# Kernel tuning notes

Hardware: AMD Instinct MI355X
Metric: run time of the kernel (lower is better)

The kernel has to match this reference:

```python
import jax, jax.numpy as jnp
import numpy as np

C = 5          # max within-cluster spike gap (module-level constant in source repo)
DELTA = 0.05   # margin constant (module-level constant in source repo)
B, T, N = 128, 512, 256


def setup_inputs() -> dict:
    key = jax.random.key(0)
    k1, k2, k3 = jax.random.split(key, 3)
    vmem = jax.random.normal(k1, (B, T, N), dtype=jnp.float32) - 1.5
    vlastmem = jax.random.normal(k2, (B, T, N), dtype=jnp.float32)  # unused by the loss math
    labels_t = jax.random.randint(k3, (B, N), 0, 4)
    ratio = jnp.float32(0.5)
    return {"vmem": vmem, "vlastmem": vlastmem, "labels_t": labels_t, "ratio": ratio}


def _per_neuron(v, key):
    """v: [T] membrane trace for one (batch, neuron). Returns (num_cluster, under_term, max_over)."""
    Tn = v.shape[0]
    t = jnp.arange(Tn)
    spike = v >= 0.0
    s = spike.astype(jnp.int32)
    # prefix sums: cs[i] = number of spikes in v[:i]
    cs = jnp.concatenate([jnp.zeros(1, jnp.int32), jnp.cumsum(s)])
    # new cluster starts at t iff spike[t] and no spike in [t-C, t-1]  (gap > C)
    prev_cnt = cs[t] - cs[jnp.clip(t - C, 0, Tn)]
    is_start = spike & (prev_cnt == 0)
    nclu = jnp.sum(is_start.astype(jnp.int32))
    # under-branch mask = union over clusters of [first-C, last+C] = C-dilation of spike train
    dil_cnt = cs[jnp.clip(t + C + 1, 0, Tn)] - cs[jnp.clip(t - C, 0, Tn)]
    mask = dil_cnt > 0

    # per-cluster stats via segmented reductions (cluster id = running count of starts)
    cid = jnp.clip(jnp.cumsum(is_start.astype(jnp.int32)) - 1, 0, Tn - 1)
    counts = jax.ops.segment_sum(s, cid, num_segments=Tn)
    first = jax.ops.segment_min(jnp.where(spike, t, Tn), cid, num_segments=Tn)
    last = jax.ops.segment_max(jnp.where(spike, t, -1), cid, num_segments=Tn)

    # over branch: cluster minimizing (end_idx - beg_idx) == min spike count (first on ties)
    counts_q = jnp.where(t < nclu, counts, Tn + 2)
    ic = jnp.argmin(counts_q)
    over_mask = (t >= first[ic]) & (t <= last[ic])
    max_over = jnp.max(jnp.where(over_mask, v, -jnp.inf))

    # under branch: if unmasked timesteps remain, penalize -max(v[mask==0]);
    # else take v at a (pinned-seed) random spike position
    has_zero = jnp.any(~mask)
    max_unmask = jnp.max(jnp.where(~mask, v, -jnp.inf))
    nsp = cs[-1]
    sorted_pos = jnp.sort(jnp.where(spike, t, Tn))
    r = jax.random.randint(key, (), 0, jnp.maximum(nsp, 1))
    v_rand = v[jnp.clip(sorted_pos[r], 0, Tn - 1)]
    under_term = jnp.where(has_zero, -max_unmask, v_rand)
    return nclu, under_term, max_over


def _forward(vmem, vlastmem, labels_t, ratio):
    Bv, Tv, Nv = vmem.shape
    vflat = jnp.swapaxes(vmem, 1, 2).reshape(Bv * Nv, Tv)   # [B*N, T]
    lflat = labels_t.reshape(Bv * Nv)
    keys = jax.random.split(jax.random.key(42), Bv * Nv)     # pinned seed for the random-spike pick
    nclu, under_term, max_over = jax.vmap(_per_neuron)(vflat, keys)
    ncf = nclu.astype(vmem.dtype)
    margin = DELTA * ratio * ncf
    under = jnp.where(lflat > nclu, under_term + margin, 0.0)
    over = jnp.where(lflat < nclu, max_over + margin, 0.0)
    loss = jnp.sum(under + over)
    spike_output = ncf.reshape(Bv, Nv)
    return loss, spike_output


def reference(vmem, vlastmem, labels_t, ratio):
    return _forward(vmem, vlastmem, labels_t, ratio)
```

## Files before the change

kernel.cpp:

```cpp
#include <hip/hip_runtime.h>
#include <stdint.h>

#define TDIM 512
#define NDIM 256
#define CGAP 5
#define DELTA_C 0.05f
#define NSEG 16
#define SEGT 32
#define BIGI (1 << 28)

extern "C" __global__ void __launch_bounds__(1024, 8)
stca_kernel(const float* __restrict__ vmem, const int* __restrict__ labels,
            const float* __restrict__ ratio_p, float* __restrict__ out,
            float* __restrict__ ws) {
  __shared__ int   si[8][NSEG * 64];
  __shared__ float sf[6][NSEG * 64];

  const int lane = threadIdx.x & 63;
  const int seg  = threadIdx.x >> 6;
  const int blk  = blockIdx.x;
  const int b    = blk >> 2;
  const int n0   = (blk & 3) << 6;
  const int n    = n0 + lane;

  const float* g = vmem + (size_t)b * TDIM * NDIM + n;
  const int t0 = seg * SEGT, t1 = t0 + SEGT;

  int   last_spike = -1000, nclu = 0, cur_cnt = 0, cur_fs = 0, fs = BIGI;
  float cur_max = -INFINITY, cur_maxlast = -INFINITY;
  float seg_run_max = -INFINITY, mfs_snap = -INFINITY;
  int   pfx_cnt = 0, pfx_ls = 0;
  float pfx_core = -INFINITY, pfx_mfs = -INFINITY;
  int   bint_cnt = BIGI;
  float bint_max = -INFINITY;
  unsigned hist = 0u;
  float umax = -INFINITY;
  float vd0 = 0.f, vd1 = 0.f, vd2 = 0.f, vd3 = 0.f, vd4 = 0.f, vd5 = 0.f;

  if (t0 > 0) {
#pragma unroll
    for (int j = 0; j < CGAP; ++j) {
      const float v = g[(size_t)(t0 - CGAP + j) * NDIM];
      hist = ((hist << 1) | (v >= 0.f ? 1u : 0u)) & 0x7FFu;
    }
  }

  auto step = [&](float v, int te) {
    const bool spike   = v >= 0.0f;
    const bool isstart = spike && ((te - last_spike) > CGAP);
    const bool closing = isstart && (nclu > 0);
    const bool isfirst = closing && (nclu == 1);
    const bool bet     = closing && (nclu > 1) && (cur_cnt < bint_cnt);
    pfx_cnt  = isfirst ? cur_cnt     : pfx_cnt;
    pfx_ls   = isfirst ? last_spike  : pfx_ls;
    pfx_core = isfirst ? cur_maxlast : pfx_core;
    pfx_mfs  = isfirst ? mfs_snap    : pfx_mfs;
    bint_cnt = bet ? cur_cnt     : bint_cnt;
    bint_max = bet ? cur_maxlast : bint_max;
    nclu += isstart ? 1 : 0;
    cur_fs  = isstart ? te : cur_fs;
    cur_max = isstart ? v : fmaxf(cur_max, v);
    cur_maxlast = spike ? cur_max : cur_maxlast;
    cur_cnt = (isstart ? 0 : cur_cnt) + (spike ? 1 : 0);
    seg_run_max = fmaxf(seg_run_max, v);
    const bool snap = spike && (nclu == 1);
    mfs_snap = snap ? seg_run_max : mfs_snap;
    fs = (spike && fs == BIGI) ? te : fs;
    last_spike = spike ? te : last_spike;
    hist = ((hist << 1) | (spike ? 1u : 0u)) & 0x7FFu;
    vd5 = vd4; vd4 = vd3; vd3 = vd2; vd2 = vd1; vd1 = vd0; vd0 = v;
    const bool un = (hist == 0u) && (te >= t0 + CGAP);
    umax = un ? fmaxf(umax, vd5) : umax;
  };

#pragma unroll 1
  for (int c = 0; c < SEGT / 8; ++c) {
    const float* gp = g + (size_t)(t0 + c * 8) * NDIM;
    const float y0 = gp[0 * NDIM], y1 = gp[1 * NDIM], y2 = gp[2 * NDIM],
                y3 = gp[3 * NDIM], y4 = gp[4 * NDIM], y5 = gp[5 * NDIM],
                y6 = gp[6 * NDIM], y7 = gp[7 * NDIM];
    const int tc = t0 + c * 8;
    step(y0, tc + 0); step(y1, tc + 1); step(y2, tc + 2); step(y3, tc + 3);
    step(y4, tc + 4); step(y5, tc + 5); step(y6, tc + 6); step(y7, tc + 7);
  }

#pragma unroll
  for (int j = 0; j < CGAP; ++j) {
    const int te = t1 + j;
    const float v = (te < TDIM) ? g[(size_t)te * NDIM] : -INFINITY;
    const bool spike = v >= 0.0f;
    hist = ((hist << 1) | (spike ? 1u : 0u)) & 0x7FFu;
    vd5 = vd4; vd4 = vd3; vd3 = vd2; vd2 = vd1; vd1 = vd0; vd0 = v;
    const bool un = (hist == 0u);
    umax = un ? fmaxf(umax, vd5) : umax;
  }

  int   sfx_cnt = 0, sfx_fs = 0;
  float sfx_core = -INFINITY, sfx_mte = -INFINITY;
  if (nclu >= 1) {
    sfx_cnt = cur_cnt; sfx_fs = cur_fs; sfx_core = cur_maxlast; sfx_mte = cur_max;
    if (nclu == 1) {
      pfx_cnt = cur_cnt; pfx_ls = last_spike; pfx_core = cur_maxlast; pfx_mfs = mfs_snap;
    }
  }

  const int idx = threadIdx.x;
  si[0][idx] = nclu;    si[1][idx] = fs;      si[2][idx] = last_spike;
  si[3][idx] = pfx_cnt; si[4][idx] = pfx_ls;  si[5][idx] = sfx_cnt;
  si[6][idx] = sfx_fs;  si[7][idx] = bint_cnt;
  sf[0][idx] = pfx_core; sf[1][idx] = pfx_mfs; sf[2][idx] = sfx_core;
  sf[3][idx] = sfx_mte;  sf[4][idx] = bint_max; sf[5][idx] = umax;
  __syncthreads();

  if (seg != 0) return;

  int   a_nclu = nclu, a_fs = fs, a_ls = last_spike;
  int   a_pcnt = pfx_cnt, a_pls = pfx_ls, a_scnt = sfx_cnt, a_sfs = sfx_fs;
  int   a_bcnt = bint_cnt;
  float a_pcore = pfx_core, a_pmfs = pfx_mfs, a_score = sfx_core, a_smte = sfx_mte;
  float a_bmax = bint_max, a_umax = umax;

  for (int s = 1; s < NSEG; ++s) {
    const int j = (s << 6) + lane;
    const int   r_nclu = si[0][j], r_fs = si[1][j], r_ls = si[2][j];
    const int   r_pcnt = si[3][j], r_pls = si[4][j];
    const int   r_scnt = si[5][j], r_sfs = si[6][j];
    const int   r_bcnt = si[7][j];
    const float r_pcore = sf[0][j], r_pmfs = sf[1][j];
    const float r_score = sf[2][j], r_smte = sf[3][j];
    const float r_bmax = sf[4][j], r_umax = sf[5][j];

    a_umax = fmaxf(a_umax, r_umax);
    if (r_nclu == 0) continue;
    if (a_nclu == 0) {
      a_nclu = r_nclu; a_fs = r_fs; a_ls = r_ls;
      a_pcnt = r_pcnt; a_pls = r_pls; a_pcore = r_pcore; a_pmfs = r_pmfs;
      a_scnt = r_scnt; a_sfs = r_sfs; a_score = r_score; a_smte = r_smte;
      a_bcnt = r_bcnt; a_bmax = r_bmax;
      continue;
    }
    if (r_fs - a_ls <= CGAP) {
      const int   Bc    = a_scnt + r_pcnt;
      const float Bcore = fmaxf(a_smte, r_pmfs);
      const float Bmfs  = fmaxf(fmaxf(a_pmfs, a_smte), r_pmfs);
      const float Bmte  = fmaxf(fmaxf(a_smte, r_pmfs), r_smte);
      const int   Bfs = a_sfs, Bls = r_pls;
      int nb = a_bcnt; float nbm = a_bmax;
      if (a_nclu >= 2 && r_nclu >= 2 && Bc < nb) { nb = Bc; nbm = Bcore; }
      if (r_bcnt < nb) { nb = r_bcnt; nbm = r_bmax; }
      if (a_nclu == 1) { a_pcnt = Bc; a_pls = Bls; a_pcore = Bcore; a_pmfs = Bmfs; }
      if (r_nclu == 1) { a_scnt = Bc; a_sfs = Bfs; a_score = Bcore; a_smte = Bmte; }
      else             { a_scnt = r_scnt; a_sfs = r_sfs; a_score = r_score; a_smte = r_smte; }
      a_bcnt = nb; a_bmax = nbm;
      a_nclu = a_nclu + r_nclu - 1;
      a_ls = r_ls;
    } else {
      int nb = a_bcnt; float nbm = a_bmax;
      if (a_nclu >= 2 && a_scnt < nb) { nb = a_scnt; nbm = a_score; }
      if (r_nclu >= 2 && r_pcnt < nb) { nb = r_pcnt; nbm = r_pcore; }
      if (r_bcnt < nb) { nb = r_bcnt; nbm = r_bmax; }
      a_bcnt = nb; a_bmax = nbm;
      a_scnt = r_scnt; a_sfs = r_sfs; a_score = r_score; a_smte = r_smte;
      a_nclu += r_nclu;
      a_ls = r_ls;
    }
  }

  int bc = a_pcnt; float bm = a_pcore;
  if (a_nclu >= 2) {
    if (a_bcnt < bc) { bc = a_bcnt; bm = a_bmax; }
    if (a_scnt < bc) { bc = a_scnt; bm = a_score; }
  }

  const float ratio = ratio_p[0];
  const int   label = labels[b * NDIM + n];
  const float ncf    = (float)a_nclu;
  const float margin = DELTA_C * ratio * ncf;
  const float under_term = (a_umax > -INFINITY) ? (-a_umax) : 0.0f;
  const float under = (label > a_nclu) ? (under_term + margin) : 0.0f;
  const float over  = (label < a_nclu) ? (bm + margin) : 0.0f;

  out[1 + b * NDIM + n] = ncf;

  float sum = under + over;
#pragma unroll
  for (int off = 32; off > 0; off >>= 1) sum += __shfl_down(sum, off);
  if (lane == 0) ws[blk] = sum;
}

extern "C" __global__ void __launch_bounds__(64, 1)
stca_reduce(const float* __restrict__ ws, float* __restrict__ out) {
  const int lane = threadIdx.x;
  float s = 0.0f;
#pragma unroll
  for (int i = 0; i < 8; ++i) s += ws[lane + (i << 6)];
#pragma unroll
  for (int off = 32; off > 0; off >>= 1) s += __shfl_down(s, off);
  if (lane == 0) out[0] = s;
}

extern "C" void kernel_launch(void* const* d_in, const int* in_sizes, int n_in,
                              void* d_out, int out_size, void* d_ws,
                              size_t ws_size, hipStream_t stream) {
  const float* vmem   = (const float*)d_in[0];
  const int*   labels = (const int*)d_in[2];
  const float* ratio  = (const float*)d_in[3];
  float* out = (float*)d_out;
  float* ws  = (float*)d_ws;

  dim3 grid(512);
  dim3 block(1024);
  hipLaunchKernelGGL(stca_kernel, grid, block, 0, stream, vmem, labels, ratio,
                     out, ws);
  hipLaunchKernelGGL(stca_reduce, dim3(1), dim3(64), 0, stream, ws, out);
}
```

Baseline: 168.5 us.

## Process two time segments per thread with interleaved independent scans

Each thread now runs two independent segment scans (A and B) with their steps interleaved, and the block shrinks from 1024 to 512 threads. The goal is more instruction-level parallelism and more loads in flight per thread on the serial dependency chain, plus less per-block shared-memory traffic and work in the merge, since segment B is merged straight from registers. The cost is higher register pressure from two scan states, which may reduce occupancy.

```diff
diff --git a/kernel.cpp b/kernel.cpp
--- a/kernel.cpp
+++ b/kernel.cpp
@@ -9,7 +9,85 @@
 #define SEGT 32
 #define BIGI (1 << 28)
 
-extern "C" __global__ void __launch_bounds__(1024, 8)
+struct Scan {
+  int   last_spike, nclu, cur_cnt, cur_fs, fs;
+  float cur_max, cur_maxlast, seg_run_max, mfs_snap;
+  int   pfx_cnt, pfx_ls;
+  float pfx_core, pfx_mfs;
+  int   bint_cnt;
+  float bint_max;
+  unsigned hist;
+  float umax;
+  float vd0, vd1, vd2, vd3, vd4, vd5;
+};
+
+__device__ __forceinline__ void scan_init(Scan& S) {
+  S.last_spike = -1000; S.nclu = 0; S.cur_cnt = 0; S.cur_fs = 0; S.fs = BIGI;
+  S.cur_max = -INFINITY; S.cur_maxlast = -INFINITY;
+  S.seg_run_max = -INFINITY; S.mfs_snap = -INFINITY;
+  S.pfx_cnt = 0; S.pfx_ls = 0; S.pfx_core = -INFINITY; S.pfx_mfs = -INFINITY;
+  S.bint_cnt = BIGI; S.bint_max = -INFINITY;
+  S.hist = 0u; S.umax = -INFINITY;
+  S.vd0 = S.vd1 = S.vd2 = S.vd3 = S.vd4 = S.vd5 = 0.f;
+}
+
+__device__ __forceinline__ void scan_step(Scan& S, float v, int te, int t0) {
+  const bool spike   = v >= 0.0f;
+  const bool isstart = spike && ((te - S.last_spike) > CGAP);
+  const bool closing = isstart && (S.nclu > 0);
+  const bool isfirst = closing && (S.nclu == 1);
+  const bool bet     = closing && (S.nclu > 1) && (S.cur_cnt < S.bint_cnt);
+  S.pfx_cnt  = isfirst ? S.cur_cnt     : S.pfx_cnt;
+  S.pfx_ls   = isfirst ? S.last_spike  : S.pfx_ls;
+  S.pfx_core = isfirst ? S.cur_maxlast : S.pfx_core;
+  S.pfx_mfs  = isfirst ? S.mfs_snap    : S.pfx_mfs;
+  S.bint_cnt = bet ? S.cur_cnt     : S.bint_cnt;
+  S.bint_max = bet ? S.cur_maxlast : S.bint_max;
+  S.nclu += isstart ? 1 : 0;
+  S.cur_fs  = isstart ? te : S.cur_fs;
+  S.cur_max = isstart ? v : fmaxf(S.cur_max, v);
+  S.cur_maxlast = spike ? S.cur_max : S.cur_maxlast;
+  S.cur_cnt = (isstart ? 0 : S.cur_cnt) + (spike ? 1 : 0);
+  S.seg_run_max = fmaxf(S.seg_run_max, v);
+  const bool snap = spike && (S.nclu == 1);
+  S.mfs_snap = snap ? S.seg_run_max : S.mfs_snap;
+  S.fs = (spike && S.fs == BIGI) ? te : S.fs;
+  S.last_spike = spike ? te : S.last_spike;
+  S.hist = ((S.hist << 1) | (spike ? 1u : 0u)) & 0x7FFu;
+  S.vd5 = S.vd4; S.vd4 = S.vd3; S.vd3 = S.vd2; S.vd2 = S.vd1; S.vd1 = S.vd0;
+  S.vd0 = v;
+  const bool un = (S.hist == 0u) && (te >= t0 + CGAP);
+  S.umax = un ? fmaxf(S.umax, S.vd5) : S.umax;
+}
+
+__device__ __forceinline__ void scan_post(Scan& S, const float* g, int t1) {
+#pragma unroll
+  for (int j = 0; j < CGAP; ++j) {
+    const int te = t1 + j;
+    const float v = (te < TDIM) ? g[(size_t)te * NDIM] : -INFINITY;
+    const bool spike = v >= 0.0f;
+    S.hist = ((S.hist << 1) | (spike ? 1u : 0u)) & 0x7FFu;
+    S.vd5 = S.vd4; S.vd4 = S.vd3; S.vd3 = S.vd2; S.vd2 = S.vd1; S.vd1 = S.vd0;
+    S.vd0 = v;
+    const bool un = (S.hist == 0u);
+    S.umax = un ? fmaxf(S.umax, S.vd5) : S.umax;
+  }
+}
+
+__device__ __forceinline__ void scan_final(Scan& S, int& sfx_cnt, int& sfx_fs,
+                                           float& sfx_core, float& sfx_mte) {
+  sfx_cnt = 0; sfx_fs = 0; sfx_core = -INFINITY; sfx_mte = -INFINITY;
+  if (S.nclu >= 1) {
+    sfx_cnt = S.cur_cnt; sfx_fs = S.cur_fs;
+    sfx_core = S.cur_maxlast; sfx_mte = S.cur_max;
+    if (S.nclu == 1) {
+      S.pfx_cnt = S.cur_cnt; S.pfx_ls = S.last_spike;
+      S.pfx_core = S.cur_maxlast; S.pfx_mfs = S.mfs_snap;
+    }
+  }
+}
+
+extern "C" __global__ void __launch_bounds__(512, 4)
 stca_kernel(const float* __restrict__ vmem, const int* __restrict__ labels,
             const float* __restrict__ ratio_p, float* __restrict__ out,
             float* __restrict__ ws) {
@@ -24,120 +102,88 @@
   const int n    = n0 + lane;
 
   const float* g = vmem + (size_t)b * TDIM * NDIM + n;
-  const int t0 = seg * SEGT, t1 = t0 + SEGT;
-
-  int   last_spike = -1000, nclu = 0, cur_cnt = 0, cur_fs = 0, fs = BIGI;
-  float cur_max = -INFINITY, cur_maxlast = -INFINITY;
-  float seg_run_max = -INFINITY, mfs_snap = -INFINITY;
-  int   pfx_cnt = 0, pfx_ls = 0;
-  float pfx_core = -INFINITY, pfx_mfs = -INFINITY;
-  int   bint_cnt = BIGI;
-  float bint_max = -INFINITY;
-  unsigned hist = 0u;
-  float umax = -INFINITY;
-  float vd0 = 0.f, vd1 = 0.f, vd2 = 0.f, vd3 = 0.f, vd4 = 0.f, vd5 = 0.f;
-
-  if (t0 > 0) {
+  const int sA = seg << 1, sB = sA + 1;
+  const int t0A = sA * SEGT, t0B = sB * SEGT;
+
+  Scan A, B;
+  scan_init(A); scan_init(B);
+
+  if (t0A > 0) {
 #pragma unroll
     for (int j = 0; j < CGAP; ++j) {
-      const float v = g[(size_t)(t0 - CGAP + j) * NDIM];
-      hist = ((hist << 1) | (v >= 0.f ? 1u : 0u)) & 0x7FFu;
-    }
-  }
-
-  auto step = [&](float v, int te) {
-    const bool spike   = v >= 0.0f;
-    const bool isstart = spike && ((te - last_spike) > CGAP);
-    const bool closing = isstart && (nclu > 0);
-    const bool isfirst = closing && (nclu == 1);
-    const bool bet     = closing && (nclu > 1) && (cur_cnt < bint_cnt);
-    pfx_cnt  = isfirst ? cur_cnt     : pfx_cnt;
-    pfx_ls   = isfirst ? last_spike  : pfx_ls;
-    pfx_core = isfirst ? cur_maxlast : pfx_core;
-    pfx_mfs  = isfirst ? mfs_snap    : pfx_mfs;
-    bint_cnt = bet ? cur_cnt     : bint_cnt;
-    bint_max = bet ? cur_maxlast : bint_max;
-    nclu += isstart ? 1 : 0;
-    cur_fs  = isstart ? te : cur_fs;
-    cur_max = isstart ? v : fmaxf(cur_max, v);
-    cur_maxlast = spike ? cur_max : cur_maxlast;
-    cur_cnt = (isstart ? 0 : cur_cnt) + (spike ? 1 : 0);
-    seg_run_max = fmaxf(seg_run_max, v);
-    const bool snap = spike && (nclu == 1);
-    mfs_snap = snap ? seg_run_max : mfs_snap;
-    fs = (spike && fs == BIGI) ? te : fs;
-    last_spike = spike ? te : last_spike;
-    hist = ((hist << 1) | (spike ? 1u : 0u)) & 0x7FFu;
-    vd5 = vd4; vd4 = vd3; vd3 = vd2; vd2 = vd1; vd1 = vd0; vd0 = v;
-    const bool un = (hist == 0u) && (te >= t0 + CGAP);
-    umax = un ? fmaxf(umax, vd5) : umax;
-  };
+      const float v = g[(size_t)(t0A - CGAP + j) * NDIM];
+      A.hist = ((A.hist << 1) | (v >= 0.f ? 1u : 0u)) & 0x7FFu;
+    }
+  }
+#pragma unroll
+  for (int j = 0; j < CGAP; ++j) {
+    const float v = g[(size_t)(t0B - CGAP + j) * NDIM];
+    B.hist = ((B.hist << 1) | (v >= 0.f ? 1u : 0u)) & 0x7FFu;
+  }
 
 #pragma unroll 1
   for (int c = 0; c < SEGT / 8; ++c) {
-    const float* gp = g + (size_t)(t0 + c * 8) * NDIM;
-    const float y0 = gp[0 * NDIM], y1 = gp[1 * NDIM], y2 = gp[2 * NDIM],
-                y3 = gp[3 * NDIM], y4 = gp[4 * NDIM], y5 = gp[5 * NDIM],
-                y6 = gp[6 * NDIM], y7 = gp[7 * NDIM];
-    const int tc = t0 + c * 8;
-    step(y0, tc + 0); step(y1, tc + 1); step(y2, tc + 2); step(y3, tc + 3);
-    step(y4, tc + 4); step(y5, tc + 5); step(y6, tc + 6); step(y7, tc + 7);
-  }
-
-#pragma unroll
-  for (int j = 0; j < CGAP; ++j) {
-    const int te = t1 + j;
-    const float v = (te < TDIM) ? g[(size_t)te * NDIM] : -INFINITY;
-    const bool spike = v >= 0.0f;
-    hist = ((hist << 1) | (spike ? 1u : 0u)) & 0x7FFu;
-    vd5 = vd4; vd4 = vd3; vd3 = vd2; vd2 = vd1; vd1 = vd0; vd0 = v;
-    const bool un = (hist == 0u);
-    umax = un ? fmaxf(umax, vd5) : umax;
-  }
-
-  int   sfx_cnt = 0, sfx_fs = 0;
-  float sfx_core = -INFINITY, sfx_mte = -INFINITY;
-  if (nclu >= 1) {
-    sfx_cnt = cur_cnt; sfx_fs = cur_fs; sfx_core = cur_maxlast; sfx_mte = cur_max;
-    if (nclu == 1) {
-      pfx_cnt = cur_cnt; pfx_ls = last_spike; pfx_core = cur_maxlast; pfx_mfs = mfs_snap;
-    }
-  }
-
-  const int idx = threadIdx.x;
-  si[0][idx] = nclu;    si[1][idx] = fs;      si[2][idx] = last_spike;
-  si[3][idx] = pfx_cnt; si[4][idx] = pfx_ls;  si[5][idx] = sfx_cnt;
-  si[6][idx] = sfx_fs;  si[7][idx] = bint_cnt;
-  sf[0][idx] = pfx_core; sf[1][idx] = pfx_mfs; sf[2][idx] = sfx_core;
-  sf[3][idx] = sfx_mte;  sf[4][idx] = bint_max; sf[5][idx] = umax;
+    const float* gpA = g + (size_t)(t0A + c * 8) * NDIM;
+    const float* gpB = g + (size_t)(t0B + c * 8) * NDIM;
+    const float y0 = gpA[0 * NDIM], y1 = gpA[1 * NDIM], y2 = gpA[2 * NDIM],
+                y3 = gpA[3 * NDIM], y4 = gpA[4 * NDIM], y5 = gpA[5 * NDIM],
+                y6 = gpA[6 * NDIM], y7 = gpA[7 * NDIM];
+    const float z0 = gpB[0 * NDIM], z1 = gpB[1 * NDIM], z2 = gpB[2 * NDIM],
+                z3 = gpB[3 * NDIM], z4 = gpB[4 * NDIM], z5 = gpB[5 * NDIM],
+                z6 = gpB[6 * NDIM], z7 = gpB[7 * NDIM];
+    const int ta = t0A + c * 8, tb = t0B + c * 8;
+    scan_step(A, y0, ta + 0, t0A); scan_step(B, z0, tb + 0, t0B);
+    scan_step(A, y1, ta + 1, t0A); scan_step(B, z1, tb + 1, t0B);
+    scan_step(A, y2, ta + 2, t0A); scan_step(B, z2, tb + 2, t0B);
+    scan_step(A, y3, ta + 3, t0A); scan_step(B, z3, tb + 3, t0B);
+    scan_step(A, y4, ta + 4, t0A); scan_step(B, z4, tb + 4, t0B);
+    scan_step(A, y5, ta + 5, t0A); scan_step(B, z5, tb + 5, t0B);
+    scan_step(A, y6, ta + 6, t0A); scan_step(B, z6, tb + 6, t0B);
+    scan_step(A, y7, ta + 7, t0A); scan_step(B, z7, tb + 7, t0B);
+  }
+
+  scan_post(A, g, t0A + SEGT);
+  scan_post(B, g, t0B + SEGT);
+
+  int sfxA_cnt, sfxA_fs; float sfxA_core, sfxA_mte;
+  int sfxB_cnt, sfxB_fs; float sfxB_core, sfxB_mte;
+  scan_final(A, sfxA_cnt, sfxA_fs, sfxA_core, sfxA_mte);
+  scan_final(B, sfxB_cnt, sfxB_fs, sfxB_core, sfxB_mte);
+
+  const int iA = (sA << 6) + lane, iB = (sB << 6) + lane;
+  si[0][iA] = A.nclu;    si[1][iA] = A.fs;      si[2][iA] = A.last_spike;
+  si[3][iA] = A.pfx_cnt; si[4][iA] = A.pfx_ls;  si[5][iA] = sfxA_cnt;
+  si[6][iA] = sfxA_fs;   si[7][iA] = A.bint_cnt;
+  sf[0][iA] = A.pfx_core; sf[1][iA] = A.pfx_mfs; sf[2][iA] = sfxA_core;
+  sf[3][iA] = sfxA_mte;   sf[4][iA] = A.bint_max; sf[5][iA] = A.umax;
+  si[0][iB] = B.nclu;    si[1][iB] = B.fs;      si[2][iB] = B.last_spike;
+  si[3][iB] = B.pfx_cnt; si[4][iB] = B.pfx_ls;  si[5][iB] = sfxB_cnt;
+  si[6][iB] = sfxB_fs;   si[7][iB] = B.bint_cnt;
+  sf[0][iB] = B.pfx_core; sf[1][iB] = B.pfx_mfs; sf[2][iB] = sfxB_core;
+  sf[3][iB] = sfxB_mte;   sf[4][iB] = B.bint_max; sf[5][iB] = B.umax;
   __syncthreads();
 
   if (seg != 0) return;
 
-  int   a_nclu = nclu, a_fs = fs, a_ls = last_spike;
-  int   a_pcnt = pfx_cnt, a_pls = pfx_ls, a_scnt = sfx_cnt, a_sfs = sfx_fs;
-  int   a_bcnt = bint_cnt;
-  float a_pcore = pfx_core, a_pmfs = pfx_mfs, a_score = sfx_core, a_smte = sfx_mte;
-  float a_bmax = bint_max, a_umax = umax;
-
-  for (int s = 1; s < NSEG; ++s) {
-    const int j = (s << 6) + lane;
-    const int   r_nclu = si[0][j], r_fs = si[1][j], r_ls = si[2][j];
-    const int   r_pcnt = si[3][j], r_pls = si[4][j];
-    const int   r_scnt = si[5][j], r_sfs = si[6][j];
-    const int   r_bcnt = si[7][j];
-    const float r_pcore = sf[0][j], r_pmfs = sf[1][j];
-    const float r_score = sf[2][j], r_smte = sf[3][j];
-    const float r_bmax = sf[4][j], r_umax = sf[5][j];
-
+  int   a_nclu = A.nclu, a_fs = A.fs, a_ls = A.last_spike;
+  int   a_pcnt = A.pfx_cnt, a_pls = A.pfx_ls, a_scnt = sfxA_cnt, a_sfs = sfxA_fs;
+  int   a_bcnt = A.bint_cnt;
+  float a_pcore = A.pfx_core, a_pmfs = A.pfx_mfs;
+  float a_score = sfxA_core, a_smte = sfxA_mte;
+  float a_bmax = A.bint_max, a_umax = A.umax;
+
+  auto merge = [&](int r_nclu, int r_fs, int r_ls, int r_pcnt, int r_pls,
+                   int r_scnt, int r_sfs, int r_bcnt,
+                   float r_pcore, float r_pmfs, float r_score, float r_smte,
+                   float r_bmax, float r_umax) {
     a_umax = fmaxf(a_umax, r_umax);
-    if (r_nclu == 0) continue;
+    if (r_nclu == 0) return;
     if (a_nclu == 0) {
       a_nclu = r_nclu; a_fs = r_fs; a_ls = r_ls;
       a_pcnt = r_pcnt; a_pls = r_pls; a_pcore = r_pcore; a_pmfs = r_pmfs;
       a_scnt = r_scnt; a_sfs = r_sfs; a_score = r_score; a_smte = r_smte;
       a_bcnt = r_bcnt; a_bmax = r_bmax;
-      continue;
+      return;
     }
     if (r_fs - a_ls <= CGAP) {
       const int   Bc    = a_scnt + r_pcnt;
@@ -164,6 +210,15 @@
       a_nclu += r_nclu;
       a_ls = r_ls;
     }
+  };
+
+  merge(B.nclu, B.fs, B.last_spike, B.pfx_cnt, B.pfx_ls, sfxB_cnt, sfxB_fs,
+        B.bint_cnt, B.pfx_core, B.pfx_mfs, sfxB_core, sfxB_mte, B.bint_max,
+        B.umax);
+  for (int s = 2; s < NSEG; ++s) {
+    const int j = (s << 6) + lane;
+    merge(si[0][j], si[1][j], si[2][j], si[3][j], si[4][j], si[5][j], si[6][j],
+          si[7][j], sf[0][j], sf[1][j], sf[2][j], sf[3][j], sf[4][j], sf[5][j]);
   }
 
   int bc = a_pcnt; float bm = a_pcore;
@@ -209,7 +264,7 @@
   float* ws  = (float*)d_ws;
 
   dim3 grid(512);
-  dim3 block(1024);
+  dim3 block(512);
   hipLaunchKernelGGL(stca_kernel, grid, block, 0, stream, vmem, labels, ratio,
                      out, ws);
   hipLaunchKernelGGL(stca_reduce, dim3(1), dim3(64), 0, stream, ws, out);
```

Result: faster. 152.2 us (-9.7%).
